# Kernel optimization log

Measured on AMD Instinct MI355X. Metric: run time of the kernel, lower is better.

Reference implementation:

```python
import jax, jax.numpy as jnp
import numpy as np
from jax import lax

H = 2048          # hidden_size
NAH = 16          # num attn heads
AHD = H // NAH    # 128
NFH = 4           # num lact (fast-weight) heads
FHD = H // NFH    # 512 = d_in = d_out
DH = FHD          # d_h = d_in * inter_multi (1.0)
WIN = 1024        # sliding window
CHUNK = 512       # lact chunk size
B, S = 2, 2048
ROPE_BASE = 500000.0
EPS = 1e-6
BASE_LR_INV = 0.001 + float(np.log(-np.expm1(-0.001)))  # inv_softplus(1e-3)


def rms_norm(x, w):
    return x * lax.rsqrt(jnp.mean(x * x, axis=-1, keepdims=True) + EPS) * w


def silu(x):
    return x * jax.nn.sigmoid(x)


def silu_backprop(dy, x):
    sg = jax.nn.sigmoid(x)
    return dy * sg * (1.0 + x * (1.0 - sg))


def apply_rope(q, k):
    # q,k: [b,s,h,d]; non-interleaved (half-split) rotary, matching flash-attn RotaryEmbedding
    d = q.shape[-1]
    inv_freq = 1.0 / (ROPE_BASE ** (jnp.arange(0, d, 2, dtype=jnp.float32) / d))
    t = jnp.arange(q.shape[1], dtype=jnp.float32)
    freqs = jnp.outer(t, inv_freq)                       # [s, d/2]
    cos = jnp.cos(freqs)[None, :, None, :]
    sin = jnp.sin(freqs)[None, :, None, :]
    def rot(x):
        x1, x2 = jnp.split(x, 2, axis=-1)
        return jnp.concatenate([x1 * cos - x2 * sin, x2 * cos + x1 * sin], axis=-1)
    return rot(q), rot(k)


def sliding_window_attn(q, k, v):
    # [b,s,h,d]; causal sliding-window attention
    s = q.shape[1]
    scale = 1.0 / np.sqrt(q.shape[-1])
    i = jnp.arange(s)[:, None]
    j = jnp.arange(s)[None, :]
    mask = (j <= i) & (i - j < WIN)                      # [s,s]
    scores = jnp.einsum('bihd,bjhd->bhij', q, k) * scale
    scores = jnp.where(mask[None, None], scores, -jnp.inf)
    p = jax.nn.softmax(scores, axis=-1)
    return jnp.einsum('bhij,bjhd->bihd', p, v)


def setup_inputs() -> dict:
    key = jax.random.key(0)
    ks = jax.random.split(key, 10)
    def n(k, shape, scale):
        return jax.random.normal(k, shape, dtype=jnp.float32) * scale
    return {
        'hidden_states': n(ks[0], (B, S, H), 1.0),
        'attn_qkv_w': n(ks[1], (3 * H, H), 0.02),
        'attn_o_w': n(ks[2], (H, H), 0.02),
        'q_norm_w': jnp.ones((H,), jnp.float32),
        'k_norm_w': jnp.ones((H,), jnp.float32),
        'mlp_norm_w': jnp.ones((H,), jnp.float32),
        'mlp_qkv_w': n(ks[3], (3 * NFH * FHD, H), 0.02),
        'mlp_o_w': n(ks[4], (H, NFH * FHD), 0.02),
        'lr_w': n(ks[5], (3 * NFH, H), 0.02),
        'lr_b': jnp.zeros((3 * NFH,), jnp.float32),
        'w0': n(ks[6], (NFH, DH, FHD), 1.0 / np.sqrt(FHD)),
        'w1': n(ks[7], (NFH, FHD, DH), 1.0 / np.sqrt(DH)),
        'w2': n(ks[8], (NFH, DH, FHD), 1.0 / np.sqrt(FHD)),
        'ttt_norm_w': jnp.ones((FHD,), jnp.float32),
    }


def _forward(hidden_states, attn_qkv_w, attn_o_w, q_norm_w, k_norm_w, mlp_norm_w,
             mlp_qkv_w, mlp_o_w, lr_w, lr_b, w0, w1, w2, ttt_norm_w):
    b, s, _ = hidden_states.shape
    # ---- sliding window attention (token mixer) ----
    qkv = hidden_states @ attn_qkv_w.T
    q, k, v = jnp.split(qkv, 3, axis=-1)
    q = rms_norm(q, q_norm_w)
    k = rms_norm(k, k_norm_w)
    q = q.reshape(b, s, NAH, AHD)
    k = k.reshape(b, s, NAH, AHD)
    v = v.reshape(b, s, NAH, AHD)
    q, k = apply_rope(q, k)
    o = sliding_window_attn(q, k, v)
    attn_out = o.reshape(b, s, H) @ attn_o_w.T

    # ---- TTT-MLP SwiGLU fast-weight channel mixer after SWA ----
    x = rms_norm(attn_out, mlp_norm_w)
    fqkv = x @ mlp_qkv_w.T
    fq, fk, fv = jnp.split(fqkv, 3, axis=-1)
    fq, fk, fv = silu(fq), silu(fk), silu(fv)
    fq = fq.reshape(b, s, NFH, FHD)
    fk = fk.reshape(b, s, NFH, FHD)
    fv = fv.reshape(b, s, NFH, FHD)
    fq = fq / jnp.clip(jnp.linalg.norm(fq, axis=-1, keepdims=True), 1e-6)
    fk = fk / jnp.clip(jnp.linalg.norm(fk, axis=-1, keepdims=True), 1e-6)

    # per-token lrs (mamba parameterization: softplus(proj + inv_softplus(base_lr)))
    lr = jax.nn.softplus(x @ lr_w.T + lr_b + BASE_LR_INV)   # [b,s,3*NFH]
    l0, l1, l2 = jnp.split(lr, 3, axis=-1)                  # each [b,s,NFH]

    nc = s // CHUNK
    def chunkify(t):  # [b,s,h,d] -> [nc,b,h,c,d]
        return t.reshape(b, nc, CHUNK, t.shape[2], t.shape[3]).transpose(1, 0, 3, 2, 4)
    qs = chunkify(fq)
    ks_ = chunkify(fk)
    vs = chunkify(fv)
    l0s = chunkify(l0[..., None])
    l1s = chunkify(l1[..., None])
    l2s = chunkify(l2[..., None])

    w0b = jnp.broadcast_to(w0[None], (b,) + w0.shape)
    w1b = jnp.broadcast_to(w1[None], (b,) + w1.shape)
    w2b = jnp.broadcast_to(w2[None], (b,) + w2.shape)

    def step(carry, inp):
        cw0, cw1, cw2 = carry
        qc, kc, vc, lr0, lr1, lr2 = inp   # qc/kc/vc: [b,h,c,d]; lr*: [b,h,c,1]
        # apply current fast weights to queries of this chunk (apply-then-update)
        gq = jnp.einsum('bhed,bhcd->bhce', cw0, qc)
        hq = silu(gq) * jnp.einsum('bhed,bhcd->bhce', cw2, qc)
        oc = jnp.einsum('bhoe,bhce->bhco', cw1, hq)
        # update fast weights with this chunk's (k, v) under negative dot-product loss
        gk = jnp.einsum('bhed,bhcd->bhce', cw0, kc)      # gate pre-act
        hbm = jnp.einsum('bhed,bhcd->bhce', cw2, kc)     # hidden before mul
        hid = silu(gk) * hbm
        dhid = jnp.einsum('bhoe,bhco->bhce', cw1, vc)    # grad wrt hidden
        dhbm = dhid * silu(gk)
        dgate = dhid * hbm
        dgpre = silu_backprop(dgate, gk)
        nw1 = cw1 + jnp.einsum('bhco,bhce->bhoe', vc * lr1, hid)
        nw0 = cw0 + jnp.einsum('bhce,bhcd->bhed', dgpre, kc * lr0)
        nw2 = cw2 + jnp.einsum('bhce,bhcd->bhed', dhbm, kc * lr2)
        return (nw0, nw1, nw2), oc

    _, ocs = lax.scan(step, (w0b, w1b, w2b), (qs, ks_, vs, l0s, l1s, l2s))
    o_fw = ocs.transpose(1, 0, 3, 2, 4).reshape(b, s, NFH, FHD)
    o_fw = rms_norm(o_fw, ttt_norm_w)
    ttt_out = o_fw.reshape(b, s, NFH * FHD) @ mlp_o_w.T
    return attn_out + ttt_out


def reference(hidden_states, attn_qkv_w, attn_o_w, q_norm_w, k_norm_w, mlp_norm_w,
              mlp_qkv_w, mlp_o_w, lr_w, lr_b, w0, w1, w2, ttt_norm_w):
    return _forward(hidden_states, attn_qkv_w, attn_o_w, q_norm_w, k_norm_w, mlp_norm_w,
                    mlp_qkv_w, mlp_o_w, lr_w, lr_b, w0, w1, w2, ttt_norm_w)
```

## Files before the change

### kernel.cpp

```cpp
#include <hip/hip_runtime.h>
#include <cmath>

typedef unsigned short u16;
typedef unsigned int u32;
typedef short s16x8 __attribute__((ext_vector_type(8)));
typedef short s16x4 __attribute__((ext_vector_type(4)));
typedef float f32x4 __attribute__((ext_vector_type(4)));

#define DEV static __device__ __forceinline__

DEV float b2f(u16 h) { return __uint_as_float(((u32)h) << 16); }
DEV u16 f2b(float f) {
  u32 u = __float_as_uint(f);
  u = (u + 0x7FFFu + ((u >> 16) & 1u)) >> 16;
  return (u16)u;
}
DEV float siluf(float x) { return x / (1.f + __expf(-x)); }

DEV void gload16(const void* g, void* l) {
  __builtin_amdgcn_global_load_lds((const __attribute__((address_space(1))) void*)g,
                                   (__attribute__((address_space(3))) void*)l, 16, 0, 0);
}

DEV s16x8 lds_frag(const u16* buf, int row, int kg) {
  int lin = row * 64 + kg * 16;
  int adr = lin ^ (((row >> 1) & 3) << 4);
  return *(const s16x8*)((const char*)buf + adr);
}

template <int MODE>
__global__ __launch_bounds__(512, 2) void gemm256(const u16* __restrict__ A, const u16* __restrict__ B,
                                                  void* __restrict__ Cout, const float* __restrict__ Cin,
                                                  int ldc, int K, int gx) {
  __shared__ __align__(16) u16 Al[4][256 * 32];
  __shared__ __align__(16) u16 Bl[4][256 * 32];
  int tid = threadIdx.x, w = tid >> 6, l = tid & 63;
  int nwg = gridDim.x;
  int wg = blockIdx.x;
  int swzb = (wg & 7) * (nwg >> 3) + (wg >> 3);
  int bx = swzb % gx, by = swzb / gx;
  const u16* Ab = A + (long)by * 256 * K;
  const u16* Bb = B + (long)bx * 256 * K;
  int wr = w >> 2, wc = w & 3;
  int fro = l & 15, kg = l >> 4;
  f32x4 acc[8][4] = {};
  int nk = K >> 5;

  auto stageA = [&](int buf, int kt) {
    #pragma unroll
    for (int i = 0; i < 2; ++i) {
      int x = (tid + i * 512) * 16;
      int y = x ^ (((x >> 7) & 3) << 4);
      gload16(Ab + (long)(y >> 6) * K + kt * 32 + ((y & 63) >> 1), (char*)&Al[buf][0] + x);
    }
  };
  auto stageB = [&](int buf, int kt) {
    #pragma unroll
    for (int i = 0; i < 2; ++i) {
      int x = (tid + i * 512) * 16;
      int y = x ^ (((x >> 7) & 3) << 4);
      gload16(Bb + (long)(y >> 6) * K + kt * 32 + ((y & 63) >> 1), (char*)&Bl[buf][0] + x);
    }
  };

  stageA(0, 0); stageB(0, 0);
  stageA(1, 1); stageB(1, 1);
  stageA(2, 2); stageB(2, 2);
  asm volatile("s_waitcnt vmcnt(8)" ::: "memory");
  __builtin_amdgcn_s_barrier();

  for (int t = 0; t < nk; ++t) {
    int cur = t & 3;
    const u16* Ac = &Al[cur][0];
    const u16* Bc = &Bl[cur][0];
    s16x8 af[8], bfr[4];
    #pragma unroll
    for (int m = 0; m < 4; ++m) af[m] = lds_frag(Ac, wr * 128 + m * 16 + fro, kg);
    #pragma unroll
    for (int n = 0; n < 4; ++n) bfr[n] = lds_frag(Bc, wc * 64 + n * 16 + fro, kg);
    if (t + 3 < nk) stageA((t + 3) & 3, t + 3);
    __builtin_amdgcn_s_barrier();
    __builtin_amdgcn_s_setprio(1);
    #pragma unroll
    for (int m = 0; m < 4; ++m)
      #pragma unroll
      for (int n = 0; n < 4; ++n)
        acc[m][n] = __builtin_amdgcn_mfma_f32_16x16x32_bf16(af[m], bfr[n], acc[m][n], 0, 0, 0);
    __builtin_amdgcn_s_setprio(0);
    __builtin_amdgcn_s_barrier();
    #pragma unroll
    for (int m = 0; m < 4; ++m) af[4 + m] = lds_frag(Ac, wr * 128 + (4 + m) * 16 + fro, kg);
    if (t + 3 < nk) stageB((t + 3) & 3, t + 3);
    __builtin_amdgcn_s_barrier();
    __builtin_amdgcn_s_setprio(1);
    #pragma unroll
    for (int m = 0; m < 4; ++m)
      #pragma unroll
      for (int n = 0; n < 4; ++n)
        acc[4 + m][n] = __builtin_amdgcn_mfma_f32_16x16x32_bf16(af[4 + m], bfr[n], acc[4 + m][n], 0, 0, 0);
    __builtin_amdgcn_s_setprio(0);
    int rem = nk - 1 - t;
    if (rem > 2)       asm volatile("s_waitcnt vmcnt(8)" ::: "memory");
    else if (rem == 2) asm volatile("s_waitcnt vmcnt(4)" ::: "memory");
    else if (rem == 1) asm volatile("s_waitcnt vmcnt(0)" ::: "memory");
    __builtin_amdgcn_s_barrier();
  }

  long rbase = (long)by * 256 + wr * 128 + kg * 4;
  long cbase = (long)bx * 256 + wc * 64 + fro;
  #pragma unroll
  for (int m = 0; m < 8; ++m)
    #pragma unroll
    for (int n = 0; n < 4; ++n)
      #pragma unroll
      for (int j = 0; j < 4; ++j) {
        long r = rbase + m * 16 + j;
        long c = cbase + n * 16;
        float v = acc[m][n][j];
        if (MODE == 2) v += Cin[r * ldc + c];
        if (MODE == 0) ((u16*)Cout)[r * ldc + c] = f2b(v);
        else ((float*)Cout)[r * ldc + c] = v;
      }
}

struct GemmDesc {
  const u16* A; const u16* B;
  float* C; const float* Cin;
  u16* Cb; u16* CbT;
  long sAb, sAh, sBb, sBh, sCb_, sCh_, sCbb, sCbh, sCtb, sCth;
  int lda, ldb, ldc, ldcb, ldct, K;
};
struct GemmBatch { GemmDesc d[5]; int nbh; };

__global__ __launch_bounds__(256) void gemm_bt(GemmBatch gb) {
  int di = blockIdx.z / gb.nbh;
  int bh = blockIdx.z % gb.nbh;
  GemmDesc d = gb.d[di];
  __shared__ __align__(16) u16 As[2][4096];
  __shared__ __align__(16) u16 Bs[2][4096];
  int tid = threadIdx.x, w = tid >> 6, l = tid & 63;
  int b2 = bh >> 2, h2 = bh & 3;
  const u16* Ab = d.A + (long)b2 * d.sAb + (long)h2 * d.sAh + (long)blockIdx.y * 128 * d.lda;
  const u16* Bb = d.B + (long)b2 * d.sBb + (long)h2 * d.sBh + (long)blockIdx.x * 128 * d.ldb;
  int srow = l >> 2, scol = (l & 3) * 8;
  f32x4 acc[4][4] = {};
  int nk = d.K >> 5;

  auto stage = [&](int buf, int kt) {
    #pragma unroll
    for (int i = 0; i < 2; ++i) {
      int chunk = i * 4 + w;
      int row = chunk * 16 + srow;
      gload16(Ab + (long)row * d.lda + kt * 32 + scol, &As[buf][chunk * 512]);
      gload16(Bb + (long)row * d.ldb + kt * 32 + scol, &Bs[buf][chunk * 512]);
    }
  };

  stage(0, 0);
  asm volatile("s_waitcnt vmcnt(0)" ::: "memory");
  __syncthreads();

  int wr = (w >> 1) * 64, wc = (w & 1) * 64;
  int fro = l & 15, fko = (l >> 4) * 8;

  for (int kt = 0; kt < nk; ++kt) {
    int buf = kt & 1;
    if (kt + 1 < nk) stage(buf ^ 1, kt + 1);
    s16x8 af[4], bfr[4];
    #pragma unroll
    for (int m = 0; m < 4; ++m) af[m] = *(const s16x8*)&As[buf][(wr + m * 16 + fro) * 32 + fko];
    #pragma unroll
    for (int n = 0; n < 4; ++n) bfr[n] = *(const s16x8*)&Bs[buf][(wc + n * 16 + fro) * 32 + fko];
    #pragma unroll
    for (int m = 0; m < 4; ++m)
      #pragma unroll
      for (int n = 0; n < 4; ++n)
        acc[m][n] = __builtin_amdgcn_mfma_f32_16x16x32_bf16(af[m], bfr[n], acc[m][n], 0, 0, 0);
    asm volatile("s_waitcnt vmcnt(0)" ::: "memory");
    __syncthreads();
  }

  float* Cp = d.C ? d.C + (long)b2 * d.sCb_ + (long)h2 * d.sCh_ : nullptr;
  const float* Ci = d.Cin ? d.Cin + (long)b2 * d.sCb_ + (long)h2 * d.sCh_ : nullptr;
  u16* Cbp = d.Cb ? d.Cb + (long)b2 * d.sCbb + (long)h2 * d.sCbh : nullptr;
  u16* Ctp = d.CbT ? d.CbT + (long)b2 * d.sCtb + (long)h2 * d.sCth : nullptr;
  long rbase = (long)blockIdx.y * 128 + wr + (l >> 4) * 4;
  long cbase = (long)blockIdx.x * 128 + wc + (l & 15);
  #pragma unroll
  for (int m = 0; m < 4; ++m)
    #pragma unroll
    for (int n = 0; n < 4; ++n)
      #pragma unroll
      for (int j = 0; j < 4; ++j) {
        long r = rbase + m * 16 + j;
        long c = cbase + n * 16;
        float v = acc[m][n][j];
        if (Ci) v += Ci[r * d.ldc + c];
        if (Cp) Cp[r * d.ldc + c] = v;
        if (Cbp) Cbp[r * d.ldcb + c] = f2b(v);
        if (Ctp) Ctp[c * d.ldct + r] = f2b(v);
      }
}

__global__ __launch_bounds__(256) void convk(const float* __restrict__ in, u16* __restrict__ outp) {
  long i = ((long)blockIdx.x * 256 + threadIdx.x) * 4;
  float4 v = *(const float4*)(in + i);
  u16 o[4] __attribute__((aligned(8))) = {f2b(v.x), f2b(v.y), f2b(v.z), f2b(v.w)};
  *(s16x4*)&outp[i] = *(const s16x4*)o;
}

__global__ __launch_bounds__(256) void norm_rope_kernel(const u16* __restrict__ qkv,
    const float* __restrict__ qw, const float* __restrict__ kw,
    u16* __restrict__ qg, u16* __restrict__ kg, u16* __restrict__ vg) {
  __shared__ float qsh[2048], ksh[2048];
  __shared__ float red[2][4];
  int t = blockIdx.x, tid = threadIdx.x, w = tid >> 6, l = tid & 63;
  int s = t & 2047;
  const u16* row = qkv + (long)t * 6144;
  s16x8 vq = *(const s16x8*)&row[tid * 8];
  s16x8 vk = *(const s16x8*)&row[2048 + tid * 8];
  float sq = 0.f, sk = 0.f;
  #pragma unroll
  for (int i = 0; i < 8; ++i) {
    float a = b2f((u16)vq[i]); qsh[tid * 8 + i] = a; sq += a * a;
    float c = b2f((u16)vk[i]); ksh[tid * 8 + i] = c; sk += c * c;
  }
  *(s16x8*)&vg[(long)t * 2048 + tid * 8] = *(const s16x8*)&row[4096 + tid * 8];
  #pragma unroll
  for (int mk = 32; mk; mk >>= 1) { sq += __shfl_xor(sq, mk, 64); sk += __shfl_xor(sk, mk, 64); }
  if (l == 0) { red[0][w] = sq; red[1][w] = sk; }
  __syncthreads();
  float rq = rsqrtf((red[0][0] + red[0][1] + red[0][2] + red[0][3]) * (1.f / 2048.f) + 1e-6f);
  float rk = rsqrtf((red[1][0] + red[1][1] + red[1][2] + red[1][3]) * (1.f / 2048.f) + 1e-6f);
  const float lf = 13.122363377404329f / 64.f;
  #pragma unroll
  for (int ii = 0; ii < 4; ++ii) {
    int pid = tid + 256 * ii;
    int h = pid >> 6, dpos = pid & 63;
    float invf = expf(-(float)dpos * lf);
    float ang = (float)s * invf;
    float sn, cs;
    sincosf(ang, &sn, &cs);
    int i1 = h * 128 + dpos, i2 = i1 + 64;
    float q1 = qsh[i1] * rq * qw[i1], q2 = qsh[i2] * rq * qw[i2];
    qg[(long)t * 2048 + i1] = f2b(q1 * cs - q2 * sn);
    qg[(long)t * 2048 + i2] = f2b(q2 * cs + q1 * sn);
    float k1 = ksh[i1] * rk * kw[i1], k2v = ksh[i2] * rk * kw[i2];
    kg[(long)t * 2048 + i1] = f2b(k1 * cs - k2v * sn);
    kg[(long)t * 2048 + i2] = f2b(k2v * cs + k1 * sn);
  }
}

__global__ __launch_bounds__(256) void vtrans_kernel(const u16* __restrict__ v, u16* __restrict__ vT) {
  __shared__ u16 T[64][74];
  int tid = threadIdx.x;
  int bh = blockIdx.z, b = bh >> 4, h = bh & 15;
  int ts = blockIdx.x * 64, dg = blockIdx.y * 64;
  int r = tid >> 2, c0 = (tid & 3) * 16;
  const u16* src = v + ((long)b * 2048 + ts + r) * 2048 + h * 128 + dg + c0;
  *(s16x8*)&T[r][c0] = *(const s16x8*)src;
  *(s16x8*)&T[r][c0 + 8] = *(const s16x8*)(src + 8);
  __syncthreads();
  int d = tid >> 2, tg = (tid & 3) * 16;
  u16 a[16] __attribute__((aligned(16)));
  #pragma unroll
  for (int j = 0; j < 16; ++j) a[j] = T[tg + j][d];
  u16* dst = vT + ((long)bh * 128 + dg + d) * 2048 + ts + tg;
  *(s16x8*)dst = ((const s16x8*)a)[0];
  *(s16x8*)(dst + 8) = ((const s16x8*)a)[1];
}

__global__ __launch_bounds__(256, 3) void attn_kernel(const u16* __restrict__ qg, const u16* __restrict__ kg,
                                                      const u16* __restrict__ vT, u16* __restrict__ og) {
  __shared__ __align__(16) u16 Ks[64][136];
  __shared__ __align__(16) u16 Vt[128][72];
  __shared__ __align__(16) u16 Ps[4][16][72];
  int tid = threadIdx.x, w = tid >> 6, l = tid & 63;
  int h = blockIdx.y, b = blockIdx.z;
  int qs = blockIdx.x * 64;
  long tokb = (long)b * 2048;
  int fr = l & 15, fg = l >> 4;
  int wrow = qs + w * 16;

  s16x8 qf[4];
  #pragma unroll
  for (int ks = 0; ks < 4; ++ks)
    qf[ks] = *(const s16x8*)&qg[(tokb + wrow + fr) * 2048 + h * 128 + ks * 32 + fg * 8];

  f32x4 oacc[8] = {};
  float mrun[4], lrun[4];
  #pragma unroll
  for (int j = 0; j < 4; ++j) { mrun[j] = -__builtin_inff(); lrun[j] = 0.f; }

  int lo = qs - 1023;
  int t0 = lo > 0 ? (lo >> 6) : 0;
  int t1 = (qs + 63) >> 6;
  const float scale = 0.088388347648318447f;

  const u16* kbase = kg + tokb * 2048 + h * 128;
  const u16* vbase = vT + (long)(b * 16 + h) * 128 * 2048;

  s16x8 kreg[4], vreg[4];
  auto loadrg = [&](int kvs) {
    #pragma unroll
    for (int it = 0; it < 4; ++it) {
      int idx = it * 256 + tid;
      kreg[it] = *(const s16x8*)&kbase[(long)(kvs + (idx >> 4)) * 2048 + (idx & 15) * 8];
      vreg[it] = *(const s16x8*)&vbase[(long)(idx >> 3) * 2048 + kvs + (idx & 7) * 8];
    }
  };
  auto writelds = [&]() {
    #pragma unroll
    for (int it = 0; it < 4; ++it) {
      int idx = it * 256 + tid;
      *(s16x8*)&Ks[idx >> 4][(idx & 15) * 8] = kreg[it];
      *(s16x8*)&Vt[idx >> 3][(idx & 7) * 8] = vreg[it];
    }
  };

  loadrg(t0 << 6);
  writelds();
  __syncthreads();

  for (int kt = t0; kt <= t1; ++kt) {
    int kvs = kt << 6;
    if (kt < t1) loadrg((kt + 1) << 6);
    bool active = (kvs <= wrow + 15);
    if (active) {
      f32x4 st[4] = {};
      #pragma unroll
      for (int ct = 0; ct < 4; ++ct)
        #pragma unroll
        for (int ks = 0; ks < 4; ++ks) {
          s16x8 kf = *(const s16x8*)&Ks[ct * 16 + fr][ks * 32 + fg * 8];
          st[ct] = __builtin_amdgcn_mfma_f32_16x16x32_bf16(qf[ks], kf, st[ct], 0, 0, 0);
        }
      bool needm = (kvs + 63 > wrow) || (kvs < wrow - 1008);
      float mx[4];
      #pragma unroll
      for (int j = 0; j < 4; ++j) mx[j] = -__builtin_inff();
      #pragma unroll
      for (int ct = 0; ct < 4; ++ct)
        #pragma unroll
        for (int j = 0; j < 4; ++j) {
          float s = st[ct][j] * scale;
          if (needm) {
            int r = wrow + fg * 4 + j;
            int c = kvs + ct * 16 + fr;
            if (c > r || (r - c) >= 1024) s = -__builtin_inff();
          }
          st[ct][j] = s;
          mx[j] = fmaxf(mx[j], s);
        }
      #pragma unroll
      for (int mk = 8; mk; mk >>= 1)
        #pragma unroll
        for (int j = 0; j < 4; ++j) mx[j] = fmaxf(mx[j], __shfl_xor(mx[j], mk, 64));
      float sc[4], nmu[4], rs[4];
      #pragma unroll
      for (int j = 0; j < 4; ++j) {
        float nm = fmaxf(mrun[j], mx[j]);
        nmu[j] = (nm == -__builtin_inff()) ? 0.f : nm;
        sc[j] = __expf(mrun[j] - nmu[j]);
        mrun[j] = nm;
        rs[j] = 0.f;
      }
      #pragma unroll
      for (int ct = 0; ct < 4; ++ct)
        #pragma unroll
        for (int j = 0; j < 4; ++j) {
          float p = __expf(st[ct][j] - nmu[j]);
          rs[j] += p;
          Ps[w][fg * 4 + j][ct * 16 + fr] = f2b(p);
        }
      #pragma unroll
      for (int mk = 8; mk; mk >>= 1)
        #pragma unroll
        for (int j = 0; j < 4; ++j) rs[j] += __shfl_xor(rs[j], mk, 64);
      #pragma unroll
      for (int j = 0; j < 4; ++j) lrun[j] = lrun[j] * sc[j] + rs[j];
      #pragma unroll
      for (int dt = 0; dt < 8; ++dt)
        #pragma unroll
        for (int j = 0; j < 4; ++j) oacc[dt][j] *= sc[j];
      #pragma unroll
      for (int kst = 0; kst < 2; ++kst) {
        s16x8 pf = *(const s16x8*)&Ps[w][fr][kst * 32 + fg * 8];
        #pragma unroll
        for (int dt = 0; dt < 8; ++dt) {
          s16x8 vf = *(const s16x8*)&Vt[dt * 16 + fr][kst * 32 + fg * 8];
          oacc[dt] = __builtin_amdgcn_mfma_f32_16x16x32_bf16(pf, vf, oacc[dt], 0, 0, 0);
        }
      }
    }
    __syncthreads();
    if (kt < t1) {
      writelds();
    }
    __syncthreads();
  }
  #pragma unroll
  for (int j = 0; j < 4; ++j) {
    float inv = 1.f / lrun[j];
    long rofs = (tokb + wrow + fg * 4 + j) * 2048 + h * 128;
    #pragma unroll
    for (int dt = 0; dt < 8; ++dt)
      og[rofs + dt * 16 + fr] = f2b(oacc[dt][j] * inv);
  }
}

__global__ __launch_bounds__(256) void rms_x_kernel(const float* __restrict__ src, const float* __restrict__ wgt,
                                                    u16* __restrict__ dst) {
  __shared__ float red[4];
  int t = blockIdx.x, tid = threadIdx.x, w = tid >> 6, l = tid & 63;
  const float* row = src + (long)t * 2048;
  float v[8] __attribute__((aligned(16)));
  ((float4*)v)[0] = *(const float4*)&row[tid * 8];
  ((float4*)v)[1] = *(const float4*)&row[tid * 8 + 4];
  float ss = 0.f;
  #pragma unroll
  for (int i = 0; i < 8; ++i) ss += v[i] * v[i];
  #pragma unroll
  for (int mk = 32; mk; mk >>= 1) ss += __shfl_xor(ss, mk, 64);
  if (l == 0) red[w] = ss;
  __syncthreads();
  float r = rsqrtf((red[0] + red[1] + red[2] + red[3]) * (1.f / 2048.f) + 1e-6f);
  #pragma unroll
  for (int i = 0; i < 8; ++i) dst[(long)t * 2048 + tid * 8 + i] = f2b(v[i] * r * wgt[tid * 8 + i]);
}

__global__ __launch_bounds__(256) void lr_kernel(const u16* __restrict__ xb, const float* __restrict__ lrw,
                                                 const float* __restrict__ lrbias, float* __restrict__ lrout,
                                                 float base) {
  __shared__ float red[4][12];
  int t = blockIdx.x, tid = threadIdx.x, w = tid >> 6, l = tid & 63;
  float xv[8];
  s16x8 rv = *(const s16x8*)&xb[(long)t * 2048 + tid * 8];
  #pragma unroll
  for (int i = 0; i < 8; ++i) xv[i] = b2f((u16)rv[i]);
  float acc[12];
  #pragma unroll
  for (int j = 0; j < 12; ++j) {
    const float4* w4 = (const float4*)(lrw + j * 2048 + tid * 8);
    float4 a = w4[0], bq = w4[1];
    acc[j] = xv[0] * a.x + xv[1] * a.y + xv[2] * a.z + xv[3] * a.w +
             xv[4] * bq.x + xv[5] * bq.y + xv[6] * bq.z + xv[7] * bq.w;
  }
  #pragma unroll
  for (int j = 0; j < 12; ++j)
    #pragma unroll
    for (int mk = 32; mk; mk >>= 1) acc[j] += __shfl_xor(acc[j], mk, 64);
  if (l == 0) {
    #pragma unroll
    for (int j = 0; j < 12; ++j) red[w][j] = acc[j];
  }
  __syncthreads();
  if (tid < 12) {
    float s_ = red[0][tid] + red[1][tid] + red[2][tid] + red[3][tid] + lrbias[tid] + base;
    lrout[(long)t * 12 + tid] = (s_ > 20.f) ? s_ : log1pf(__expf(s_));
  }
}

__global__ __launch_bounds__(256) void silu_norm_kernel(const u16* __restrict__ fqkv,
    u16* __restrict__ fqo, u16* __restrict__ fko, u16* __restrict__ fvo) {
  int t = blockIdx.x, tid = threadIdx.x, w = tid >> 6, l = tid & 63;
  const u16* row = fqkv + (long)t * 6144;
  {
    s16x8 rv = *(const s16x8*)&row[w * 512 + l * 8];
    float x[8]; float ss = 0.f;
    #pragma unroll
    for (int i = 0; i < 8; ++i) { x[i] = siluf(b2f((u16)rv[i])); ss += x[i] * x[i]; }
    #pragma unroll
    for (int mk = 32; mk; mk >>= 1) ss += __shfl_xor(ss, mk, 64);
    float sc = 1.f / fmaxf(sqrtf(ss), 1e-6f);
    #pragma unroll
    for (int i = 0; i < 8; ++i) fqo[(long)t * 2048 + w * 512 + l * 8 + i] = f2b(x[i] * sc);
  }
  {
    s16x8 rv = *(const s16x8*)&row[2048 + w * 512 + l * 8];
    float x[8]; float ss = 0.f;
    #pragma unroll
    for (int i = 0; i < 8; ++i) { x[i] = siluf(b2f((u16)rv[i])); ss += x[i] * x[i]; }
    #pragma unroll
    for (int mk = 32; mk; mk >>= 1) ss += __shfl_xor(ss, mk, 64);
    float sc = 1.f / fmaxf(sqrtf(ss), 1e-6f);
    #pragma unroll
    for (int i = 0; i < 8; ++i) fko[(long)t * 2048 + w * 512 + l * 8 + i] = f2b(x[i] * sc);
  }
  {
    s16x8 rv = *(const s16x8*)&row[4096 + tid * 8];
    #pragma unroll
    for (int i = 0; i < 8; ++i) fvo[(long)t * 2048 + tid * 8 + i] = f2b(siluf(b2f((u16)rv[i])));
  }
}

__global__ __launch_bounds__(256) void winit_kernel(const float* __restrict__ w0, const float* __restrict__ w1,
                                                    const float* __restrict__ w2,
                                                    float* __restrict__ wbuf0, u16* __restrict__ wb16) {
  long gid = (long)blockIdx.x * 256 + threadIdx.x;
  long e4 = gid * 4;
  int which = (int)(e4 >> 21);
  long rem = e4 & 2097151L;
  int bh = (int)(rem >> 18);
  long idx = rem & 262143L;
  int h = bh & 3;
  const float* src = (which == 0 ? w0 : which == 1 ? w1 : w2) + (long)h * 262144 + idx;
  float4 v = *(const float4*)src;
  *(float4*)(wbuf0 + e4) = v;
  u16 o[4] __attribute__((aligned(8))) = {f2b(v.x), f2b(v.y), f2b(v.z), f2b(v.w)};
  *(s16x4*)&wb16[e4] = *(const s16x4*)o;
  if (which == 1) {
    u16* wt = wb16 + 3L * 2097152 + (long)bh * 262144;
    int r = (int)(idx >> 9), c = (int)(idx & 511);
    wt[(long)(c + 0) * 512 + r] = o[0];
    wt[(long)(c + 1) * 512 + r] = o[1];
    wt[(long)(c + 2) * 512 + r] = o[2];
    wt[(long)(c + 3) * 512 + r] = o[3];
  }
}

__global__ __launch_bounds__(256) void ttt_elem_kernel(
    const float* __restrict__ t5, u16* __restrict__ hqb,
    u16* __restrict__ hidT, u16* __restrict__ dhbmT, u16* __restrict__ dgpT,
    const u16* __restrict__ fk, const u16* __restrict__ fv, const float* __restrict__ lr,
    u16* __restrict__ k0T, u16* __restrict__ k2T, u16* __restrict__ v1T, int ic) {
  __shared__ u16 T0[64][72], T1[64][72], T2[64][72];
  int tid = threadIdx.x;
  int bh = blockIdx.y, b = bh >> 2, h = bh & 3;
  int tc = (blockIdx.x >> 3) * 64, te = (blockIdx.x & 7) * 64;
  int r = tid >> 2, c0 = (tid & 3) * 16;
  long base = (long)bh * 262144 + (long)(tc + r) * 512 + te + c0;

  {
    float gq_[16] __attribute__((aligned(16)));
    float q2_[16] __attribute__((aligned(16)));
    const float* pgq = t5 + base;
    const float* pq2 = t5 + 2097152L + base;
    #pragma unroll
    for (int q4 = 0; q4 < 4; ++q4) {
      ((float4*)gq_)[q4] = *(const float4*)(pgq + q4 * 4);
      ((float4*)q2_)[q4] = *(const float4*)(pq2 + q4 * 4);
    }
    u16 hq_[16] __attribute__((aligned(16)));
    #pragma unroll
    for (int i = 0; i < 16; ++i) hq_[i] = f2b(siluf(gq_[i]) * q2_[i]);
    *(s16x8*)&hqb[base] = ((const s16x8*)hq_)[0];
    *(s16x8*)&hqb[base + 8] = ((const s16x8*)hq_)[1];
  }
  {
    float gk_[16] __attribute__((aligned(16)));
    float k2_[16] __attribute__((aligned(16)));
    float dh_[16] __attribute__((aligned(16)));
    const float* pgk = t5 + 2L * 2097152 + base;
    const float* pk2 = t5 + 3L * 2097152 + base;
    const float* pdh = t5 + 4L * 2097152 + base;
    #pragma unroll
    for (int q4 = 0; q4 < 4; ++q4) {
      ((float4*)gk_)[q4] = *(const float4*)(pgk + q4 * 4);
      ((float4*)k2_)[q4] = *(const float4*)(pk2 + q4 * 4);
      ((float4*)dh_)[q4] = *(const float4*)(pdh + q4 * 4);
    }
    #pragma unroll
    for (int i = 0; i < 16; ++i) {
      float sg = 1.f / (1.f + __expf(-gk_[i]));
      float sil = gk_[i] * sg;
      float hid = sil * k2_[i];
      float dhbm = dh_[i] * sil;
      float dgate = dh_[i] * k2_[i];
      float dgp = dgate * sg * (1.f + gk_[i] * (1.f - sg));
      T0[r][c0 + i] = f2b(hid);
      T1[r][c0 + i] = f2b(dhbm);
      T2[r][c0 + i] = f2b(dgp);
    }
  }
  __syncthreads();
  long obase = (long)bh * 262144 + (long)(te + r) * 512 + tc + c0;
  {
    u16 a0[16] __attribute__((aligned(16))), a1[16] __attribute__((aligned(16))), a2[16] __attribute__((aligned(16)));
    #pragma unroll
    for (int i = 0; i < 16; ++i) { a0[i] = T0[c0 + i][r]; a1[i] = T1[c0 + i][r]; a2[i] = T2[c0 + i][r]; }
    *(s16x8*)&hidT[obase] = ((const s16x8*)a0)[0];   *(s16x8*)&hidT[obase + 8] = ((const s16x8*)a0)[1];
    *(s16x8*)&dhbmT[obase] = ((const s16x8*)a1)[0];  *(s16x8*)&dhbmT[obase + 8] = ((const s16x8*)a1)[1];
    *(s16x8*)&dgpT[obase] = ((const s16x8*)a2)[0];   *(s16x8*)&dgpT[obase + 8] = ((const s16x8*)a2)[1];
  }
  __syncthreads();
  {
    long to = (long)b * 2048 + (long)ic * 512 + tc + r;
    float l0 = lr[to * 12 + h], l1 = lr[to * 12 + 4 + h], l2 = lr[to * 12 + 8 + h];
    long goff = to * 2048 + (long)h * 512 + te + c0;
    s16x8 ka = *(const s16x8*)&fk[goff];
    s16x8 kb8 = *(const s16x8*)&fk[goff + 8];
    s16x8 va = *(const s16x8*)&fv[goff];
    s16x8 vb8 = *(const s16x8*)&fv[goff + 8];
    #pragma unroll
    for (int i = 0; i < 8; ++i) {
      float kv1 = b2f((u16)ka[i]), kv2 = b2f((u16)kb8[i]);
      float vv1 = b2f((u16)va[i]), vv2 = b2f((u16)vb8[i]);
      T0[r][c0 + i] = f2b(kv1 * l0);      T0[r][c0 + 8 + i] = f2b(kv2 * l0);
      T1[r][c0 + i] = f2b(kv1 * l2);      T1[r][c0 + 8 + i] = f2b(kv2 * l2);
      T2[r][c0 + i] = f2b(vv1 * l1);      T2[r][c0 + 8 + i] = f2b(vv2 * l1);
    }
  }
  __syncthreads();
  {
    u16 a0[16] __attribute__((aligned(16))), a1[16] __attribute__((aligned(16))), a2[16] __attribute__((aligned(16)));
    #pragma unroll
    for (int i = 0; i < 16; ++i) { a0[i] = T0[c0 + i][r]; a1[i] = T1[c0 + i][r]; a2[i] = T2[c0 + i][r]; }
    *(s16x8*)&k0T[obase] = ((const s16x8*)a0)[0];  *(s16x8*)&k0T[obase + 8] = ((const s16x8*)a0)[1];
    *(s16x8*)&k2T[obase] = ((const s16x8*)a1)[0];  *(s16x8*)&k2T[obase + 8] = ((const s16x8*)a1)[1];
    *(s16x8*)&v1T[obase] = ((const s16x8*)a2)[0];  *(s16x8*)&v1T[obase + 8] = ((const s16x8*)a2)[1];
  }
}

__global__ __launch_bounds__(256) void ttt_norm_kernel(const u16* __restrict__ src, const float* __restrict__ wgt,
                                                       u16* __restrict__ dst) {
  int t = blockIdx.x, tid = threadIdx.x, w = tid >> 6, l = tid & 63;
  long off = (long)t * 2048 + w * 512 + l * 8;
  s16x8 rv = *(const s16x8*)&src[off];
  float x[8];
  float ss = 0.f;
  #pragma unroll
  for (int i = 0; i < 8; ++i) { x[i] = b2f((u16)rv[i]); ss += x[i] * x[i]; }
  #pragma unroll
  for (int mk = 32; mk; mk >>= 1) ss += __shfl_xor(ss, mk, 64);
  float r = rsqrtf(ss * (1.f / 512.f) + 1e-6f);
  #pragma unroll
  for (int i = 0; i < 8; ++i) dst[off + i] = f2b(x[i] * r * wgt[l * 8 + i]);
}

extern "C" void kernel_launch(void* const* d_in, const int* in_sizes, int n_in,
                              void* d_out, int out_size, void* d_ws, size_t ws_size,
                              hipStream_t stream) {
  const float* hidden     = (const float*)d_in[0];
  const float* attn_qkv_w = (const float*)d_in[1];
  const float* attn_o_w   = (const float*)d_in[2];
  const float* q_norm_w   = (const float*)d_in[3];
  const float* k_norm_w   = (const float*)d_in[4];
  const float* mlp_norm_w = (const float*)d_in[5];
  const float* mlp_qkv_w  = (const float*)d_in[6];
  const float* mlp_o_w    = (const float*)d_in[7];
  const float* lr_w       = (const float*)d_in[8];
  const float* lr_bias    = (const float*)d_in[9];
  const float* w0in       = (const float*)d_in[10];
  const float* w1in       = (const float*)d_in[11];
  const float* w2in       = (const float*)d_in[12];
  const float* ttt_w      = (const float*)d_in[13];
  float* out = (float*)d_out;

  char* ws = (char*)d_ws;
  u16* hbf   = (u16*)(ws + 0);
  u16* wqb   = (u16*)(ws + 16777216);
  u16* wob   = (u16*)(ws + 41943040);
  char* big  = ws + 50331648;
  u16* qbuf  = (u16*)(ws + 121634816);
  u16* kbuf  = (u16*)(ws + 138412032);
  u16* vbuf  = (u16*)(ws + 155189248);
  u16* obuf  = (u16*)(ws + 171966464);
  float* lrb_ = (float*)(ws + 188743680);
  float* wbuf = (float*)(ws + 188940288);
  u16* wb16  = (u16*)(ws + 239271936);

  u16* qkvb = (u16*)big;
  u16* vTb  = (u16*)(big + 50331648);
  float* t5 = (float*)big;
  u16* hqb   = (u16*)(big + 41943040);
  u16* hidT  = (u16*)(big + 46137344);
  u16* dhbmT = (u16*)(big + 50331648);
  u16* dgpT  = (u16*)(big + 54525952);
  u16* k0T   = (u16*)(big + 58720256);
  u16* k2T   = (u16*)(big + 62914560);
  u16* v1T   = (u16*)(big + 67108864);
  u16* xb  = hbf;
  u16* ofw = hbf;

  convk<<<8192, 256, 0, stream>>>(hidden, hbf);
  convk<<<12288, 256, 0, stream>>>(attn_qkv_w, wqb);
  convk<<<4096, 256, 0, stream>>>(attn_o_w, wob);

  gemm256<0><<<384, 512, 0, stream>>>(hbf, wqb, qkvb, nullptr, 6144, 2048, 24);
  norm_rope_kernel<<<4096, 256, 0, stream>>>(qkvb, q_norm_w, k_norm_w, qbuf, kbuf, vbuf);
  vtrans_kernel<<<dim3(32, 2, 32), 256, 0, stream>>>(vbuf, vTb);
  attn_kernel<<<dim3(32, 16, 2), 256, 0, stream>>>(qbuf, kbuf, vTb, obuf);
  gemm256<1><<<128, 512, 0, stream>>>(obuf, wob, out, nullptr, 2048, 2048, 8);
  rms_x_kernel<<<4096, 256, 0, stream>>>(out, mlp_norm_w, xb);
  convk<<<12288, 256, 0, stream>>>(mlp_qkv_w, wqb);
  convk<<<4096, 256, 0, stream>>>(mlp_o_w, wob);
  float base_lr_inv = 0.001f + logf(-expm1f(-0.001f));
  lr_kernel<<<4096, 256, 0, stream>>>(xb, lr_w, lr_bias, lrb_, base_lr_inv);
  gemm256<0><<<384, 512, 0, stream>>>(xb, wqb, qkvb, nullptr, 6144, 2048, 24);
  silu_norm_kernel<<<4096, 256, 0, stream>>>(qkvb, qbuf, kbuf, vbuf);
  winit_kernel<<<6144, 256, 0, stream>>>(w0in, w1in, w2in, wbuf, wb16);

  for (int ic = 0; ic < 4; ++ic) {
    {
      GemmBatch g{}; g.nbh = 8;
      const u16* Asrc[5] = {qbuf, qbuf, kbuf, kbuf, vbuf};
      long Bwhich[5] = {0, 2, 0, 2, 3};
      for (int i = 0; i < 5; ++i) {
        GemmDesc& dd = g.d[i];
        dd.A = Asrc[i] + (long)ic * 1048576; dd.sAb = 4194304; dd.sAh = 512; dd.lda = 2048;
        dd.B = wb16 + Bwhich[i] * 2097152;   dd.sBb = 1048576; dd.sBh = 262144; dd.ldb = 512;
        dd.C = t5 + (long)i * 2097152;       dd.sCb_ = 1048576; dd.sCh_ = 262144; dd.ldc = 512;
        dd.K = 512;
      }
      gemm_bt<<<dim3(4, 4, 40), 256, 0, stream>>>(g);
    }
    ttt_elem_kernel<<<dim3(64, 8), 256, 0, stream>>>(t5, hqb, hidT, dhbmT, dgpT,
                                                     kbuf, vbuf, lrb_, k0T, k2T, v1T, ic);
    {
      GemmBatch g{}; g.nbh = 8;
      GemmDesc& dd = g.d[0];
      dd.A = hqb; dd.sAb = 1048576; dd.sAh = 262144; dd.lda = 512;
      dd.B = wb16 + 2097152; dd.sBb = 1048576; dd.sBh = 262144; dd.ldb = 512;
      dd.Cb = ofw + (long)ic * 1048576; dd.sCbb = 4194304; dd.sCbh = 512; dd.ldcb = 2048;
      dd.K = 512;
      gemm_bt<<<dim3(4, 4, 8), 256, 0, stream>>>(g);
    }
    {
      GemmBatch g{}; g.nbh = 8;
      float* wc_ = wbuf + (long)(ic & 1) * 6291456;
      float* wn_ = wbuf + (long)((ic & 1) ^ 1) * 6291456;
      const u16* A3[3] = {dgpT, v1T, dhbmT};
      const u16* B3[3] = {k0T, hidT, k2T};
      for (int i = 0; i < 3; ++i) {
        GemmDesc& dd = g.d[i];
        dd.A = A3[i]; dd.sAb = 1048576; dd.sAh = 262144; dd.lda = 512;
        dd.B = B3[i]; dd.sBb = 1048576; dd.sBh = 262144; dd.ldb = 512;
        dd.Cin = wc_ + (long)i * 2097152; dd.C = wn_ + (long)i * 2097152;
        dd.sCb_ = 1048576; dd.sCh_ = 262144; dd.ldc = 512;
        dd.Cb = wb16 + (long)i * 2097152; dd.sCbb = 1048576; dd.sCbh = 262144; dd.ldcb = 512;
        if (i == 1) { dd.CbT = wb16 + 3L * 2097152; dd.sCtb = 1048576; dd.sCth = 262144; dd.ldct = 512; }
        dd.K = 512;
      }
      gemm_bt<<<dim3(4, 4, 24), 256, 0, stream>>>(g);
    }
  }
  ttt_norm_kernel<<<4096, 256, 0, stream>>>(ofw, ttt_w, obuf);
  gemm256<2><<<128, 512, 0, stream>>>(obuf, wob, out, out, 2048, 2048, 8);
  (void)in_sizes; (void)n_in; (void)out_size; (void)ws_size;
}
```

Baseline: 1.061 ms.

## Replace 256x256 dense GEMM with 128x128 tiles and triple-buffered pipeline

Replaces the 256x256-tile, 512-thread GEMM with a 128x128-tile, 256-thread kernel that has three LDS buffers and a prefetch distance of two, and changes the workgroup-to-tile swizzle. The O-projection GEMMs previously launched only 128 workgroups on a GPU with many more compute units, so smaller tiles are meant to fill the machine and improve occupancy. The cost is lower data reuse per tile and more global and LDS traffic for the large QKV GEMMs. The loop also becomes simpler, with one sync point per k-step.

```diff
diff --git a/kernel.cpp b/kernel.cpp
--- a/kernel.cpp
+++ b/kernel.cpp
@@ -29,57 +29,51 @@
 }
 
 template <int MODE>
-__global__ __launch_bounds__(512, 2) void gemm256(const u16* __restrict__ A, const u16* __restrict__ B,
+__global__ __launch_bounds__(256, 3) void gemm128(const u16* __restrict__ A, const u16* __restrict__ B,
                                                   void* __restrict__ Cout, const float* __restrict__ Cin,
                                                   int ldc, int K, int gx) {
-  __shared__ __align__(16) u16 Al[4][256 * 32];
-  __shared__ __align__(16) u16 Bl[4][256 * 32];
+  __shared__ __align__(16) u16 Al[3][128 * 32];
+  __shared__ __align__(16) u16 Bl[3][128 * 32];
   int tid = threadIdx.x, w = tid >> 6, l = tid & 63;
-  int nwg = gridDim.x;
-  int wg = blockIdx.x;
-  int swzb = (wg & 7) * (nwg >> 3) + (wg >> 3);
-  int bx = swzb % gx, by = swzb / gx;
-  const u16* Ab = A + (long)by * 256 * K;
-  const u16* Bb = B + (long)bx * 256 * K;
-  int wr = w >> 2, wc = w & 3;
+  int cpx = gx >> 3;
+  int idx = blockIdx.x >> 3;
+  int bx = (blockIdx.x & 7) * cpx + idx % cpx;
+  int by = idx / cpx;
+  const u16* Ab = A + (long)by * 128 * K;
+  const u16* Bb = B + (long)bx * 128 * K;
+  int wr = w >> 1, wc = w & 1;
   int fro = l & 15, kg = l >> 4;
-  f32x4 acc[8][4] = {};
+  f32x4 acc[4][4] = {};
   int nk = K >> 5;
 
-  auto stageA = [&](int buf, int kt) {
+  auto stage = [&](int buf, int kt) {
     #pragma unroll
     for (int i = 0; i < 2; ++i) {
-      int x = (tid + i * 512) * 16;
+      int x = (tid + i * 256) * 16;
       int y = x ^ (((x >> 7) & 3) << 4);
       gload16(Ab + (long)(y >> 6) * K + kt * 32 + ((y & 63) >> 1), (char*)&Al[buf][0] + x);
+      gload16(Bb + (long)(y >> 6) * K + kt * 32 + ((y & 63) >> 1), (char*)&Bl[buf][0] + x);
     }
   };
-  auto stageB = [&](int buf, int kt) {
-    #pragma unroll
-    for (int i = 0; i < 2; ++i) {
-      int x = (tid + i * 512) * 16;
-      int y = x ^ (((x >> 7) & 3) << 4);
-      gload16(Bb + (long)(y >> 6) * K + kt * 32 + ((y & 63) >> 1), (char*)&Bl[buf][0] + x);
-    }
-  };
-
-  stageA(0, 0); stageB(0, 0);
-  stageA(1, 1); stageB(1, 1);
-  stageA(2, 2); stageB(2, 2);
-  asm volatile("s_waitcnt vmcnt(8)" ::: "memory");
+
+  stage(0, 0);
+  stage(1, 1);
+  asm volatile("s_waitcnt vmcnt(4)" ::: "memory");
   __builtin_amdgcn_s_barrier();
 
+  int cur = 0;
   for (int t = 0; t < nk; ++t) {
-    int cur = t & 3;
     const u16* Ac = &Al[cur][0];
     const u16* Bc = &Bl[cur][0];
-    s16x8 af[8], bfr[4];
-    #pragma unroll
-    for (int m = 0; m < 4; ++m) af[m] = lds_frag(Ac, wr * 128 + m * 16 + fro, kg);
+    s16x8 af[4], bfr[4];
+    #pragma unroll
+    for (int m = 0; m < 4; ++m) af[m] = lds_frag(Ac, wr * 64 + m * 16 + fro, kg);
     #pragma unroll
     for (int n = 0; n < 4; ++n) bfr[n] = lds_frag(Bc, wc * 64 + n * 16 + fro, kg);
-    if (t + 3 < nk) stageA((t + 3) & 3, t + 3);
-    __builtin_amdgcn_s_barrier();
+    if (t + 2 < nk) {
+      int nb = cur + 2; if (nb >= 3) nb -= 3;
+      stage(nb, t + 2);
+    }
     __builtin_amdgcn_s_setprio(1);
     #pragma unroll
     for (int m = 0; m < 4; ++m)
@@ -87,29 +81,16 @@
       for (int n = 0; n < 4; ++n)
         acc[m][n] = __builtin_amdgcn_mfma_f32_16x16x32_bf16(af[m], bfr[n], acc[m][n], 0, 0, 0);
     __builtin_amdgcn_s_setprio(0);
+    if (t + 2 < nk)      asm volatile("s_waitcnt vmcnt(4)" ::: "memory");
+    else if (t + 1 < nk) asm volatile("s_waitcnt vmcnt(0)" ::: "memory");
     __builtin_amdgcn_s_barrier();
-    #pragma unroll
-    for (int m = 0; m < 4; ++m) af[4 + m] = lds_frag(Ac, wr * 128 + (4 + m) * 16 + fro, kg);
-    if (t + 3 < nk) stageB((t + 3) & 3, t + 3);
-    __builtin_amdgcn_s_barrier();
-    __builtin_amdgcn_s_setprio(1);
-    #pragma unroll
-    for (int m = 0; m < 4; ++m)
-      #pragma unroll
-      for (int n = 0; n < 4; ++n)
-        acc[4 + m][n] = __builtin_amdgcn_mfma_f32_16x16x32_bf16(af[4 + m], bfr[n], acc[4 + m][n], 0, 0, 0);
-    __builtin_amdgcn_s_setprio(0);
-    int rem = nk - 1 - t;
-    if (rem > 2)       asm volatile("s_waitcnt vmcnt(8)" ::: "memory");
-    else if (rem == 2) asm volatile("s_waitcnt vmcnt(4)" ::: "memory");
-    else if (rem == 1) asm volatile("s_waitcnt vmcnt(0)" ::: "memory");
-    __builtin_amdgcn_s_barrier();
-  }
-
-  long rbase = (long)by * 256 + wr * 128 + kg * 4;
-  long cbase = (long)bx * 256 + wc * 64 + fro;
-  #pragma unroll
-  for (int m = 0; m < 8; ++m)
+    if (++cur == 3) cur = 0;
+  }
+
+  long rbase = (long)by * 128 + wr * 64 + kg * 4;
+  long cbase = (long)bx * 128 + wc * 64 + fro;
+  #pragma unroll
+  for (int m = 0; m < 4; ++m)
     #pragma unroll
     for (int n = 0; n < 4; ++n)
       #pragma unroll
@@ -677,17 +658,17 @@
   convk<<<12288, 256, 0, stream>>>(attn_qkv_w, wqb);
   convk<<<4096, 256, 0, stream>>>(attn_o_w, wob);
 
-  gemm256<0><<<384, 512, 0, stream>>>(hbf, wqb, qkvb, nullptr, 6144, 2048, 24);
+  gemm128<0><<<1536, 256, 0, stream>>>(hbf, wqb, qkvb, nullptr, 6144, 2048, 48);
   norm_rope_kernel<<<4096, 256, 0, stream>>>(qkvb, q_norm_w, k_norm_w, qbuf, kbuf, vbuf);
   vtrans_kernel<<<dim3(32, 2, 32), 256, 0, stream>>>(vbuf, vTb);
   attn_kernel<<<dim3(32, 16, 2), 256, 0, stream>>>(qbuf, kbuf, vTb, obuf);
-  gemm256<1><<<128, 512, 0, stream>>>(obuf, wob, out, nullptr, 2048, 2048, 8);
+  gemm128<1><<<512, 256, 0, stream>>>(obuf, wob, out, nullptr, 2048, 2048, 16);
   rms_x_kernel<<<4096, 256, 0, stream>>>(out, mlp_norm_w, xb);
   convk<<<12288, 256, 0, stream>>>(mlp_qkv_w, wqb);
   convk<<<4096, 256, 0, stream>>>(mlp_o_w, wob);
   float base_lr_inv = 0.001f + logf(-expm1f(-0.001f));
   lr_kernel<<<4096, 256, 0, stream>>>(xb, lr_w, lr_bias, lrb_, base_lr_inv);
-  gemm256<0><<<384, 512, 0, stream>>>(xb, wqb, qkvb, nullptr, 6144, 2048, 24);
+  gemm128<0><<<1536, 256, 0, stream>>>(xb, wqb, qkvb, nullptr, 6144, 2048, 48);
   silu_norm_kernel<<<4096, 256, 0, stream>>>(qkvb, qbuf, kbuf, vbuf);
   winit_kernel<<<6144, 256, 0, stream>>>(w0in, w1in, w2in, wbuf, wb16);
 
@@ -736,6 +717,6 @@
     }
   }
   ttt_norm_kernel<<<4096, 256, 0, stream>>>(ofw, ttt_w, obuf);
-  gemm256<2><<<128, 512, 0, stream>>>(obuf, wob, out, out, 2048, 2048, 8);
+  gemm128<2><<<512, 256, 0, stream>>>(obuf, wob, out, out, 2048, 2048, 16);
   (void)in_sizes; (void)n_in; (void)out_size; (void)ws_size;
 }
```

After: 994.3 us. 1.07x faster.
